# Kernel tuning notes

Hardware: AMD Instinct MI355X
Metric: run time of the kernel (lower is better)

The kernel has to match this reference:

```python
import jax, jax.numpy as jnp
import numpy as np

N = 100000   # nodes
E = 500000   # edges per relation
D = 128      # in_dim == out_dim
R = 3        # relations
NEG_SLOPE = 0.2  # DGL GATConv default


def setup_inputs() -> dict:
    key = jax.random.key(0)
    ks = jax.random.split(key, 7)
    x = jax.random.normal(ks[0], (N, D), jnp.float32)
    src = jax.random.randint(ks[1], (R, E), 0, N, jnp.int32)
    dst = jax.random.randint(ks[2], (R, E), 0, N, jnp.int32)
    W = jax.random.normal(ks[3], (R, D, D), jnp.float32) * 0.05
    attn_l = jax.random.normal(ks[4], (R, D), jnp.float32) * 0.05
    attn_r = jax.random.normal(ks[5], (R, D), jnp.float32) * 0.05
    bias = jnp.zeros((R, D), jnp.float32)
    return {"x": x, "src": src, "dst": dst, "W": W,
            "attn_l": attn_l, "attn_r": attn_r, "bias": bias}


def _gat_rel(x, src, dst, W, al, ar, b):
    # GATConv, num_heads=1: project, per-edge attention, segment softmax over dst
    feat = x @ W.T                                   # [N, D]
    el = (feat * al).sum(-1)                         # [N]
    er = (feat * ar).sum(-1)                         # [N]
    e = jax.nn.leaky_relu(el[src] + er[dst], NEG_SLOPE)   # [E]
    m = jax.ops.segment_max(e, dst, num_segments=N)       # stable softmax max per dst
    ex = jnp.exp(e - m[dst])
    s = jax.ops.segment_sum(ex, dst, num_segments=N)
    alpha = ex / s[dst]                                    # edge softmax weights
    out = jax.ops.segment_sum(alpha[:, None] * feat[src], dst, num_segments=N)
    return out + b                                         # GATConv bias


def reference(x, src, dst, W, attn_l, attn_r, bias):
    # HeteroGraphConv(aggregate='mean') over relations, then squeeze(head dim)
    outs = [_gat_rel(x, src[r], dst[r], W[r], attn_l[r], attn_r[r], bias[r])
            for r in range(R)]
    return jnp.mean(jnp.stack(outs, axis=0), axis=0)
```

## Files before the change

kernel.cpp:

```cpp
#include <hip/hip_runtime.h>
#include <hip/hip_bf16.h>

#define NN 100000
#define DD 128
#define RR 3
#define EE 500000
#define CAP 44
#define BK 196
#define ECAP 8192
#define SELR 50176

using bf16 = __hip_bfloat16;
typedef __attribute__((ext_vector_type(8))) short short8;
typedef __attribute__((ext_vector_type(4))) float f32x4;

__device__ __forceinline__ unsigned short f2bf(float f) {
  unsigned int u = __float_as_uint(f);
  return (unsigned short)((u + 0x7fffu + ((u >> 16) & 1u)) >> 16);
}
__device__ __forceinline__ float blo(unsigned int u) { return __uint_as_float(u << 16); }
__device__ __forceinline__ float bhi(unsigned int u) { return __uint_as_float(u & 0xffff0000u); }

__device__ __forceinline__ void ld_lds16(const void* g, void* l) {
  __builtin_amdgcn_global_load_lds((const __attribute__((address_space(1))) unsigned int*)g,
                                   (__attribute__((address_space(3))) unsigned int*)l, 16, 0, 0);
}

__global__ __launch_bounds__(256) void k_prepw(
    const float* __restrict__ W, const float* __restrict__ bias,
    short* __restrict__ Wb, float* __restrict__ bm)
{
  int idx = blockIdx.x * 256 + threadIdx.x;
  float4 v = ((const float4*)W)[idx];
  short4 s;
  s.x = (short)f2bf(v.x); s.y = (short)f2bf(v.y);
  s.z = (short)f2bf(v.z); s.w = (short)f2bf(v.w);
  ((short4*)Wb)[idx] = s;
  if (blockIdx.x == 0 && threadIdx.x < DD) {
    int t = threadIdx.x;
    bm[t] = (bias[t] + bias[DD + t] + bias[2 * DD + t]) * (1.f / 3.f);
  }
}

__global__ __launch_bounds__(256, 2) void k_gemm(
    const float* __restrict__ x, const short* __restrict__ Wb,
    const float* __restrict__ attn_l, const float* __restrict__ attn_r,
    short* __restrict__ feat, float* __restrict__ el, float* __restrict__ er)
{
  __shared__ __align__(16) char smem[65536];
  const int t = threadIdx.x, lane = t & 63, wave = t >> 6;
  const int row0 = blockIdx.x * 128;
  const int ml = lane & 15, q = lane >> 4;
  const int wr = wave >> 1, wc = wave & 1;

  {
    const int rbase = t >> 5, c4 = t & 31;
    const int chunk = c4 >> 1, half = c4 & 1;
    const int dst0 = ((chunk ^ (rbase & 7)) << 4) + (half << 3);
    const float4* x4 = (const float4*)x;
#pragma unroll 4
    for (int i = 0; i < 16; ++i) {
      int row = i * 8 + rbase;
      int grow = row0 + row; if (grow >= NN) grow = NN - 1;
      float4 v = x4[(size_t)grow * 32 + c4];
      unsigned int p0 = ((unsigned int)f2bf(v.y) << 16) | f2bf(v.x);
      unsigned int p1 = ((unsigned int)f2bf(v.w) << 16) | f2bf(v.z);
      *(uint2*)(smem + row * 256 + dst0) = make_uint2(p0, p1);
    }
  }

  int mbase[4], nbase[4];
#pragma unroll
  for (int i = 0; i < 4; ++i) {
    mbase[i] = (wr * 64 + i * 16 + ml) * 256;
    nbase[i] = 32768 + (wc * 64 + i * 16 + ml) * 256;
  }

  for (int rel = 0; rel < RR; ++rel) {
    if (rel) __syncthreads();
    {
      const int rloc = q & 3;
#pragma unroll
      for (int i = 0; i < 8; ++i) {
        int rowB = wave * 32 + i * 4 + rloc;
        int c = ml ^ (rowB & 7);
        const short* gp = Wb + (size_t)(rel * 128 + rowB) * 128 + c * 8;
        ld_lds16(gp, smem + 32768 + wave * 8192 + i * 1024);
      }
    }
    __syncthreads();

    f32x4 acc[4][4] = {};
#pragma unroll
    for (int kc = 0; kc < 4; ++kc) {
      const int sw = ((kc * 4 + q) ^ (ml & 7)) << 4;
      short8 av[4], bv[4];
#pragma unroll
      for (int i = 0; i < 4; ++i) av[i] = *(const short8*)(smem + mbase[i] + sw);
#pragma unroll
      for (int i = 0; i < 4; ++i) bv[i] = *(const short8*)(smem + nbase[i] + sw);
#pragma unroll
      for (int mi = 0; mi < 4; ++mi)
#pragma unroll
        for (int ni = 0; ni < 4; ++ni)
          acc[mi][ni] = __builtin_amdgcn_mfma_f32_16x16x32_bf16(av[mi], bv[ni], acc[mi][ni], 0, 0, 0);
    }

    float pel[4][4], per_[4][4];
    {
      float alv[4], arv[4];
#pragma unroll
      for (int ni = 0; ni < 4; ++ni) {
        int c = rel * DD + wc * 64 + ni * 16 + ml;
        alv[ni] = attn_l[c]; arv[ni] = attn_r[c];
      }
#pragma unroll
      for (int mi = 0; mi < 4; ++mi)
#pragma unroll
        for (int reg = 0; reg < 4; ++reg) {
          float se = 0.f, sr = 0.f;
#pragma unroll
          for (int ni = 0; ni < 4; ++ni) {
            se = fmaf(acc[mi][ni][reg], alv[ni], se);
            sr = fmaf(acc[mi][ni][reg], arv[ni], sr);
          }
          pel[mi][reg] = se; per_[mi][reg] = sr;
        }
#pragma unroll
      for (int msk = 1; msk < 16; msk <<= 1)
#pragma unroll
        for (int mi = 0; mi < 4; ++mi)
#pragma unroll
          for (int reg = 0; reg < 4; ++reg) {
            pel[mi][reg]  += __shfl_xor(pel[mi][reg], msk);
            per_[mi][reg] += __shfl_xor(per_[mi][reg], msk);
          }
    }

    char* fb = (char*)feat + (size_t)rel * NN * 256;
#pragma unroll
    for (int p = 0; p < 2; ++p) {
      __syncthreads();
      if (p == 0 && ml == 0) {
#pragma unroll
        for (int mi = 0; mi < 4; ++mi)
#pragma unroll
          for (int reg = 0; reg < 4; ++reg) {
            int row = wr * 64 + mi * 16 + q * 4 + reg;
            *(float*)(smem + SELR + row * 16 + wc * 4)     = pel[mi][reg];
            *(float*)(smem + SELR + row * 16 + 8 + wc * 4) = per_[mi][reg];
          }
      }
      if (wr == p) {
#pragma unroll
        for (int mi = 0; mi < 4; ++mi)
#pragma unroll
          for (int ni = 0; ni < 4; ++ni) {
            f32x4 v = acc[mi][ni];
#pragma unroll
            for (int reg = 0; reg < 4; ++reg) {
              int rl = mi * 16 + q * 4 + reg;
              *(short*)(smem + 32768 + rl * 272 + wc * 128 + ni * 32 + ml * 2) = (short)f2bf(v[reg]);
            }
          }
      }
      __syncthreads();
      if (p == 0 && t < 128 && row0 + t < NN) {
        float4 v = *(const float4*)(smem + SELR + t * 16);
        el[rel * NN + row0 + t] = v.x + v.y;
        er[rel * NN + row0 + t] = v.z + v.w;
      }
#pragma unroll
      for (int o = 0; o < 4; ++o) {
        int rl = o * 16 + (t >> 4);
        int coloff = (t & 15) * 16;
        int grow = row0 + p * 64 + rl;
        if (grow < NN) {
          int4 v = *(const int4*)(smem + 32768 + rl * 272 + coloff);
          *(int4*)(fb + (size_t)grow * 256 + coloff) = v;
        }
      }
    }
  }
}

__global__ __launch_bounds__(256) void k_part(
    const int* __restrict__ src, const int* __restrict__ dst,
    int* __restrict__ gcur, int* __restrict__ ebuf)
{
  __shared__ int lh[BK];
  const int t = threadIdx.x;
  for (int b = t; b < BK; b += 256) lh[b] = 0;
  __syncthreads();

  int eb[8], ebk[8];
  const int base = blockIdx.x * 2048 + t;
#pragma unroll
  for (int k = 0; k < 8; ++k) {
    int i = base + k * 256;
    ebk[k] = -1;
    if (i < RR * EE) {
      int d = __builtin_nontemporal_load(&dst[i]);
      int s = __builtin_nontemporal_load(&src[i]);
      int r = i >= 2 * EE ? 2 : (i >= EE ? 1 : 0);
      ebk[k] = d >> 9;
      eb[k] = ((d & 511) << 19) | (r << 17) | s;
      atomicAdd(&lh[ebk[k]], 1);
    }
  }
  __syncthreads();
  if (t < BK) {
    int v = lh[t];
    lh[t] = v ? atomicAdd(&gcur[t], v) : 0;
  }
  __syncthreads();
#pragma unroll
  for (int k = 0; k < 8; ++k) {
    if (ebk[k] >= 0) {
      int pos = atomicAdd(&lh[ebk[k]], 1);
      if (pos < ECAP) ebuf[ebk[k] * ECAP + pos] = eb[k];
    }
  }
}

__global__ __launch_bounds__(256) void k_build(
    const int* __restrict__ gcur, const int* __restrict__ ebuf,
    int* __restrict__ counts, int* __restrict__ payload)
{
  __shared__ int lcnt[512];
  const int b = blockIdx.x, t = threadIdx.x;
  lcnt[t] = 0; lcnt[t + 256] = 0;
  __syncthreads();
  int cnt = gcur[b]; if (cnt > ECAP) cnt = ECAP;
  const int n0 = b << 9;
  for (int i = t; i < cnt; i += 256) {
    int ent = ebuf[b * ECAP + i];
    int dlow = ent >> 19;
    int pos = atomicAdd(&lcnt[dlow], 1);
    if (pos < CAP)
      payload[(size_t)(n0 + dlow) * CAP + pos] = ((ent >> 17) & 3) * NN + (ent & 0x1FFFF);
  }
  __syncthreads();
  if (n0 + t < NN)       counts[n0 + t] = lcnt[t];
  if (n0 + t + 256 < NN) counts[n0 + t + 256] = lcnt[t + 256];
}

__global__ __launch_bounds__(256) void k_gather(
    const int* __restrict__ counts, const int* __restrict__ payload,
    const float* __restrict__ el, const float* __restrict__ er,
    const short* __restrict__ feat, const float* __restrict__ bm,
    float* __restrict__ out)
{
  const int lane = threadIdx.x & 63;
  const int hw = lane >> 4, m = lane & 15;
  const int n = blockIdx.x * 4 + (threadIdx.x >> 6);
  int deg = counts[n];
  deg = deg > CAP ? CAP : deg;
  const float er0 = er[n], er1 = er[NN + n], er2 = er[2 * NN + n];
  const bool act = lane < deg;
  int pl = act ? payload[(size_t)n * CAP + lane] : 0;
  int r = pl >= 2 * NN ? 2 : (pl >= NN ? 1 : 0);
  float ex = 0.f;
  if (act) {
    float e = el[pl] + (r == 0 ? er0 : (r == 1 ? er1 : er2));
    e = e >= 0.f ? e : 0.2f * e;
    ex = __expf(e);
  }
  float v0 = (act && r == 0) ? ex : 0.f;
  float v1 = (act && r == 1) ? ex : 0.f;
  float v2 = (act && r == 2) ? ex : 0.f;
#pragma unroll
  for (int msk = 1; msk < 64; msk <<= 1) {
    v0 += __shfl_xor(v0, msk);
    v1 += __shfl_xor(v1, msk);
    v2 += __shfl_xor(v2, msk);
  }
  float i0 = v0 > 0.f ? 1.f / v0 : 0.f;
  float i1 = v1 > 0.f ? 1.f / v1 : 0.f;
  float i2 = v2 > 0.f ? 1.f / v2 : 0.f;
  float w = ex * (r == 0 ? i0 : (r == 1 ? i1 : i2));

  float a8[8] = {0.f, 0.f, 0.f, 0.f, 0.f, 0.f, 0.f, 0.f};
  const unsigned short* fs = (const unsigned short*)feat;
  for (int e = 0; e < deg; e += 8) {
#pragma unroll
    for (int g = 0; g < 2; ++g) {
      int idx = e + g * 4 + hw;
      float we = __shfl(w, idx);
      int pe = __shfl(pl, idx);
      uint4 u = *(const uint4*)(fs + (size_t)pe * DD + m * 8);
      a8[0] = fmaf(we, blo(u.x), a8[0]); a8[1] = fmaf(we, bhi(u.x), a8[1]);
      a8[2] = fmaf(we, blo(u.y), a8[2]); a8[3] = fmaf(we, bhi(u.y), a8[3]);
      a8[4] = fmaf(we, blo(u.z), a8[4]); a8[5] = fmaf(we, bhi(u.z), a8[5]);
      a8[6] = fmaf(we, blo(u.w), a8[6]); a8[7] = fmaf(we, bhi(u.w), a8[7]);
    }
  }
#pragma unroll
  for (int k = 0; k < 8; ++k) {
    a8[k] += __shfl_xor(a8[k], 16);
    a8[k] += __shfl_xor(a8[k], 32);
  }
  if (hw == 0) {
    const int j = m * 8;
    float4 b0 = *(const float4*)(bm + j);
    float4 b1 = *(const float4*)(bm + j + 4);
    float4 o0, o1;
    o0.x = a8[0] * (1.f / 3.f) + b0.x; o0.y = a8[1] * (1.f / 3.f) + b0.y;
    o0.z = a8[2] * (1.f / 3.f) + b0.z; o0.w = a8[3] * (1.f / 3.f) + b0.w;
    o1.x = a8[4] * (1.f / 3.f) + b1.x; o1.y = a8[5] * (1.f / 3.f) + b1.y;
    o1.z = a8[6] * (1.f / 3.f) + b1.z; o1.w = a8[7] * (1.f / 3.f) + b1.w;
    float* op = out + (size_t)n * DD + j;
    *(float4*)op = o0;
    *(float4*)(op + 4) = o1;
  }
}

extern "C" void kernel_launch(void* const* d_in, const int* in_sizes, int n_in,
                              void* d_out, int out_size, void* d_ws, size_t ws_size,
                              hipStream_t stream)
{
  const float* x    = (const float*)d_in[0];
  const int*   src  = (const int*)d_in[1];
  const int*   dst  = (const int*)d_in[2];
  const float* W    = (const float*)d_in[3];
  const float* al   = (const float*)d_in[4];
  const float* ar   = (const float*)d_in[5];
  const float* bias = (const float*)d_in[6];
  float* out = (float*)d_out;

  char* p = (char*)d_ws;
  short* feat    = (short*)p; p += (size_t)RR * NN * DD * 2;
  int*   payload = (int*)p;   p += (size_t)NN * CAP * 4;
  int*   ebuf    = (int*)p;   p += (size_t)BK * ECAP * 4;
  float* el      = (float*)p; p += (size_t)RR * NN * 4;
  float* er      = (float*)p; p += (size_t)RR * NN * 4;
  short* Wb      = (short*)p; p += (size_t)RR * DD * DD * 2;
  float* bm      = (float*)p; p += (size_t)DD * 4;
  int*   counts  = (int*)p;   p += (size_t)NN * 4;
  int*   gcur    = (int*)p;   p += (size_t)BK * 4;

  hipMemsetAsync(gcur, 0, (size_t)BK * 4, stream);
  k_prepw<<<48, 256, 0, stream>>>(W, bias, Wb, bm);
  k_gemm<<<(NN + 127) / 128, 256, 0, stream>>>(x, Wb, al, ar, feat, el, er);
  k_part<<<(RR * EE + 2047) / 2048, 256, 0, stream>>>(src, dst, gcur, ebuf);
  k_build<<<BK, 256, 0, stream>>>(gcur, ebuf, counts, payload);
  k_gather<<<NN / 4, 256, 0, stream>>>(counts, payload, el, er, feat, bm, out);
}
```

Baseline: 266.3 us.

## Fuse GEMM and edge partition into one launch and fold memset into prep

Merges the projection GEMM and the edge bucketing kernel into a single launch, with block indices splitting the work between the two bodies, so independent work can overlap on the GPU. The gcur zeroing moves from a separate memset into the weight-prep kernel. This removes two launches and the idle tail between kernels. In exchange, partition blocks now carry the GEMM's 64KB shared allocation and launch bounds, which may lower their occupancy.

```diff
diff --git a/kernel.cpp b/kernel.cpp
--- a/kernel.cpp
+++ b/kernel.cpp
@@ -9,6 +9,8 @@
 #define BK 196
 #define ECAP 8192
 #define SELR 50176
+#define GEMM_NB 782
+#define PART_NB 733
 
 using bf16 = __hip_bfloat16;
 typedef __attribute__((ext_vector_type(8))) short short8;
@@ -26,9 +28,9 @@
                                    (__attribute__((address_space(3))) unsigned int*)l, 16, 0, 0);
 }
 
-__global__ __launch_bounds__(256) void k_prepw(
+__global__ __launch_bounds__(256) void k_pre(
     const float* __restrict__ W, const float* __restrict__ bias,
-    short* __restrict__ Wb, float* __restrict__ bm)
+    short* __restrict__ Wb, float* __restrict__ bm, int* __restrict__ gcur)
 {
   int idx = blockIdx.x * 256 + threadIdx.x;
   float4 v = ((const float4*)W)[idx];
@@ -40,16 +42,17 @@
     int t = threadIdx.x;
     bm[t] = (bias[t] + bias[DD + t] + bias[2 * DD + t]) * (1.f / 3.f);
   }
-}
-
-__global__ __launch_bounds__(256, 2) void k_gemm(
+  if (blockIdx.x == 1 && threadIdx.x < BK) gcur[threadIdx.x] = 0;
+}
+
+__device__ __forceinline__ void gemm_body(
+    char* smem, int bid,
     const float* __restrict__ x, const short* __restrict__ Wb,
     const float* __restrict__ attn_l, const float* __restrict__ attn_r,
     short* __restrict__ feat, float* __restrict__ el, float* __restrict__ er)
 {
-  __shared__ __align__(16) char smem[65536];
   const int t = threadIdx.x, lane = t & 63, wave = t >> 6;
-  const int row0 = blockIdx.x * 128;
+  const int row0 = bid * 128;
   const int ml = lane & 15, q = lane >> 4;
   const int wr = wave >> 1, wc = wave & 1;
 
@@ -184,17 +187,18 @@
   }
 }
 
-__global__ __launch_bounds__(256) void k_part(
+__device__ __forceinline__ void part_body(
+    char* smem, int vb,
     const int* __restrict__ src, const int* __restrict__ dst,
     int* __restrict__ gcur, int* __restrict__ ebuf)
 {
-  __shared__ int lh[BK];
+  int* lh = (int*)smem;
   const int t = threadIdx.x;
   for (int b = t; b < BK; b += 256) lh[b] = 0;
   __syncthreads();
 
   int eb[8], ebk[8];
-  const int base = blockIdx.x * 2048 + t;
+  const int base = vb * 2048 + t;
 #pragma unroll
   for (int k = 0; k < 8; ++k) {
     int i = base + k * 256;
@@ -220,6 +224,21 @@
       int pos = atomicAdd(&lh[ebk[k]], 1);
       if (pos < ECAP) ebuf[ebk[k] * ECAP + pos] = eb[k];
     }
+  }
+}
+
+__global__ __launch_bounds__(256, 2) void k_fused(
+    const float* __restrict__ x, const short* __restrict__ Wb,
+    const float* __restrict__ attn_l, const float* __restrict__ attn_r,
+    short* __restrict__ feat, float* __restrict__ el, float* __restrict__ er,
+    const int* __restrict__ src, const int* __restrict__ dst,
+    int* __restrict__ gcur, int* __restrict__ ebuf)
+{
+  __shared__ __align__(16) char smem[65536];
+  if (blockIdx.x < GEMM_NB) {
+    gemm_body(smem, blockIdx.x, x, Wb, attn_l, attn_r, feat, el, er);
+  } else {
+    part_body(smem, blockIdx.x - GEMM_NB, src, dst, gcur, ebuf);
   }
 }
 
@@ -339,10 +358,9 @@
   int*   counts  = (int*)p;   p += (size_t)NN * 4;
   int*   gcur    = (int*)p;   p += (size_t)BK * 4;
 
-  hipMemsetAsync(gcur, 0, (size_t)BK * 4, stream);
-  k_prepw<<<48, 256, 0, stream>>>(W, bias, Wb, bm);
-  k_gemm<<<(NN + 127) / 128, 256, 0, stream>>>(x, Wb, al, ar, feat, el, er);
-  k_part<<<(RR * EE + 2047) / 2048, 256, 0, stream>>>(src, dst, gcur, ebuf);
+  k_pre<<<48, 256, 0, stream>>>(W, bias, Wb, bm, gcur);
+  k_fused<<<GEMM_NB + PART_NB, 256, 0, stream>>>(x, Wb, al, ar, feat, el, er,
+                                                 src, dst, gcur, ebuf);
   k_build<<<BK, 256, 0, stream>>>(gcur, ebuf, counts, payload);
   k_gather<<<NN / 4, 256, 0, stream>>>(counts, payload, el, er, feat, bm, out);
 }
```

New measurement: 246.6 us. 1.08x faster.

## Aggregate raw x per relation before projecting, folding attention into weights

Applied to the files above, without the earlier changes.

Reorders the computation so each destination first aggregates raw fp32 x rows per relation (softmax weights per relation segment) into a bf16 buffer, then a single GEMM applies W over the three relations and adds the bias. The attention logits el/er come from precomputed W^T·attn vectors, which removes the initial projection GEMM. The el/er computation is fused with edge partitioning in one launch, gcur zeroing moves into the prep kernel, and the build kernel sorts edges by relation within each node. The gather now reads fp32 x rows (twice the bytes of the old bf16 feat) and writes a 3×N×D bf16 intermediate, trading gather bandwidth for fewer kernels and less GEMM work.

```diff
diff --git a/kernel.cpp b/kernel.cpp
--- a/kernel.cpp
+++ b/kernel.cpp
@@ -8,9 +8,10 @@
 #define CAP 44
 #define BK 196
 #define ECAP 8192
-#define SELR 50176
-
-using bf16 = __hip_bfloat16;
+#define GEMM_NB 782
+#define PART_NB 733
+#define PRE2_NB 256
+
 typedef __attribute__((ext_vector_type(8))) short short8;
 typedef __attribute__((ext_vector_type(4))) float f32x4;
 
@@ -18,17 +19,12 @@
   unsigned int u = __float_as_uint(f);
   return (unsigned short)((u + 0x7fffu + ((u >> 16) & 1u)) >> 16);
 }
-__device__ __forceinline__ float blo(unsigned int u) { return __uint_as_float(u << 16); }
-__device__ __forceinline__ float bhi(unsigned int u) { return __uint_as_float(u & 0xffff0000u); }
-
-__device__ __forceinline__ void ld_lds16(const void* g, void* l) {
-  __builtin_amdgcn_global_load_lds((const __attribute__((address_space(1))) unsigned int*)g,
-                                   (__attribute__((address_space(3))) unsigned int*)l, 16, 0, 0);
-}
-
-__global__ __launch_bounds__(256) void k_prepw(
+
+__global__ __launch_bounds__(256) void k_pre(
     const float* __restrict__ W, const float* __restrict__ bias,
-    short* __restrict__ Wb, float* __restrict__ bm)
+    const float* __restrict__ al, const float* __restrict__ ar,
+    short* __restrict__ Wb, float* __restrict__ bm,
+    float* __restrict__ wal, float* __restrict__ war, int* __restrict__ gcur)
 {
   int idx = blockIdx.x * 256 + threadIdx.x;
   float4 v = ((const float4*)W)[idx];
@@ -40,161 +36,75 @@
     int t = threadIdx.x;
     bm[t] = (bias[t] + bias[DD + t] + bias[2 * DD + t]) * (1.f / 3.f);
   }
-}
-
-__global__ __launch_bounds__(256, 2) void k_gemm(
-    const float* __restrict__ x, const short* __restrict__ Wb,
-    const float* __restrict__ attn_l, const float* __restrict__ attn_r,
-    short* __restrict__ feat, float* __restrict__ el, float* __restrict__ er)
-{
-  __shared__ __align__(16) char smem[65536];
-  const int t = threadIdx.x, lane = t & 63, wave = t >> 6;
-  const int row0 = blockIdx.x * 128;
-  const int ml = lane & 15, q = lane >> 4;
-  const int wr = wave >> 1, wc = wave & 1;
-
-  {
-    const int rbase = t >> 5, c4 = t & 31;
-    const int chunk = c4 >> 1, half = c4 & 1;
-    const int dst0 = ((chunk ^ (rbase & 7)) << 4) + (half << 3);
-    const float4* x4 = (const float4*)x;
-#pragma unroll 4
-    for (int i = 0; i < 16; ++i) {
-      int row = i * 8 + rbase;
-      int grow = row0 + row; if (grow >= NN) grow = NN - 1;
-      float4 v = x4[(size_t)grow * 32 + c4];
-      unsigned int p0 = ((unsigned int)f2bf(v.y) << 16) | f2bf(v.x);
-      unsigned int p1 = ((unsigned int)f2bf(v.w) << 16) | f2bf(v.z);
-      *(uint2*)(smem + row * 256 + dst0) = make_uint2(p0, p1);
-    }
-  }
-
-  int mbase[4], nbase[4];
-#pragma unroll
-  for (int i = 0; i < 4; ++i) {
-    mbase[i] = (wr * 64 + i * 16 + ml) * 256;
-    nbase[i] = 32768 + (wc * 64 + i * 16 + ml) * 256;
-  }
-
-  for (int rel = 0; rel < RR; ++rel) {
-    if (rel) __syncthreads();
-    {
-      const int rloc = q & 3;
-#pragma unroll
-      for (int i = 0; i < 8; ++i) {
-        int rowB = wave * 32 + i * 4 + rloc;
-        int c = ml ^ (rowB & 7);
-        const short* gp = Wb + (size_t)(rel * 128 + rowB) * 128 + c * 8;
-        ld_lds16(gp, smem + 32768 + wave * 8192 + i * 1024);
+  if (blockIdx.x == 1 && threadIdx.x < BK) gcur[threadIdx.x] = 0;
+  if (blockIdx.x == 2 && threadIdx.x < DD) {
+    int d = threadIdx.x;
+    float accl[RR] = {0.f, 0.f, 0.f}, accr[RR] = {0.f, 0.f, 0.f};
+    for (int i = 0; i < DD; ++i) {
+#pragma unroll
+      for (int r = 0; r < RR; ++r) {
+        float wv = W[(size_t)r * DD * DD + i * DD + d];
+        accl[r] = fmaf(wv, al[r * DD + i], accl[r]);
+        accr[r] = fmaf(wv, ar[r * DD + i], accr[r]);
       }
     }
-    __syncthreads();
-
-    f32x4 acc[4][4] = {};
-#pragma unroll
-    for (int kc = 0; kc < 4; ++kc) {
-      const int sw = ((kc * 4 + q) ^ (ml & 7)) << 4;
-      short8 av[4], bv[4];
-#pragma unroll
-      for (int i = 0; i < 4; ++i) av[i] = *(const short8*)(smem + mbase[i] + sw);
-#pragma unroll
-      for (int i = 0; i < 4; ++i) bv[i] = *(const short8*)(smem + nbase[i] + sw);
-#pragma unroll
-      for (int mi = 0; mi < 4; ++mi)
-#pragma unroll
-        for (int ni = 0; ni < 4; ++ni)
-          acc[mi][ni] = __builtin_amdgcn_mfma_f32_16x16x32_bf16(av[mi], bv[ni], acc[mi][ni], 0, 0, 0);
-    }
-
-    float pel[4][4], per_[4][4];
-    {
-      float alv[4], arv[4];
-#pragma unroll
-      for (int ni = 0; ni < 4; ++ni) {
-        int c = rel * DD + wc * 64 + ni * 16 + ml;
-        alv[ni] = attn_l[c]; arv[ni] = attn_r[c];
+#pragma unroll
+    for (int r = 0; r < RR; ++r) { wal[r * DD + d] = accl[r]; war[r * DD + d] = accr[r]; }
+  }
+}
+
+__device__ __forceinline__ void pre2_body(
+    int vb, const float* __restrict__ x,
+    const float* __restrict__ wal, const float* __restrict__ war,
+    float* __restrict__ el, float* __restrict__ er)
+{
+  const int t = threadIdx.x;
+  const int rowslot = t >> 5, lane32 = t & 31;
+  float4 wl[RR], wr2[RR];
+#pragma unroll
+  for (int r = 0; r < RR; ++r) {
+    wl[r]  = *(const float4*)(wal + r * DD + lane32 * 4);
+    wr2[r] = *(const float4*)(war + r * DD + lane32 * 4);
+  }
+  const int rpb = (NN + PRE2_NB - 1) / PRE2_NB;
+  int rbeg = vb * rpb;
+  int rend = rbeg + rpb; if (rend > NN) rend = NN;
+  for (int row = rbeg + rowslot; row < rend; row += 8) {
+    float4 xv = *(const float4*)(x + (size_t)row * DD + lane32 * 4);
+    float pl_[RR], pr_[RR];
+#pragma unroll
+    for (int r = 0; r < RR; ++r) {
+      pl_[r] = fmaf(xv.w, wl[r].w, fmaf(xv.z, wl[r].z, fmaf(xv.y, wl[r].y, xv.x * wl[r].x)));
+      pr_[r] = fmaf(xv.w, wr2[r].w, fmaf(xv.z, wr2[r].z, fmaf(xv.y, wr2[r].y, xv.x * wr2[r].x)));
+    }
+#pragma unroll
+    for (int msk = 1; msk < 32; msk <<= 1)
+#pragma unroll
+      for (int r = 0; r < RR; ++r) {
+        pl_[r] += __shfl_xor(pl_[r], msk);
+        pr_[r] += __shfl_xor(pr_[r], msk);
       }
-#pragma unroll
-      for (int mi = 0; mi < 4; ++mi)
-#pragma unroll
-        for (int reg = 0; reg < 4; ++reg) {
-          float se = 0.f, sr = 0.f;
-#pragma unroll
-          for (int ni = 0; ni < 4; ++ni) {
-            se = fmaf(acc[mi][ni][reg], alv[ni], se);
-            sr = fmaf(acc[mi][ni][reg], arv[ni], sr);
-          }
-          pel[mi][reg] = se; per_[mi][reg] = sr;
-        }
-#pragma unroll
-      for (int msk = 1; msk < 16; msk <<= 1)
-#pragma unroll
-        for (int mi = 0; mi < 4; ++mi)
-#pragma unroll
-          for (int reg = 0; reg < 4; ++reg) {
-            pel[mi][reg]  += __shfl_xor(pel[mi][reg], msk);
-            per_[mi][reg] += __shfl_xor(per_[mi][reg], msk);
-          }
-    }
-
-    char* fb = (char*)feat + (size_t)rel * NN * 256;
-#pragma unroll
-    for (int p = 0; p < 2; ++p) {
-      __syncthreads();
-      if (p == 0 && ml == 0) {
-#pragma unroll
-        for (int mi = 0; mi < 4; ++mi)
-#pragma unroll
-          for (int reg = 0; reg < 4; ++reg) {
-            int row = wr * 64 + mi * 16 + q * 4 + reg;
-            *(float*)(smem + SELR + row * 16 + wc * 4)     = pel[mi][reg];
-            *(float*)(smem + SELR + row * 16 + 8 + wc * 4) = per_[mi][reg];
-          }
+    if (lane32 == 0) {
+#pragma unroll
+      for (int r = 0; r < RR; ++r) {
+        el[r * NN + row] = pl_[r];
+        er[r * NN + row] = pr_[r];
       }
-      if (wr == p) {
-#pragma unroll
-        for (int mi = 0; mi < 4; ++mi)
-#pragma unroll
-          for (int ni = 0; ni < 4; ++ni) {
-            f32x4 v = acc[mi][ni];
-#pragma unroll
-            for (int reg = 0; reg < 4; ++reg) {
-              int rl = mi * 16 + q * 4 + reg;
-              *(short*)(smem + 32768 + rl * 272 + wc * 128 + ni * 32 + ml * 2) = (short)f2bf(v[reg]);
-            }
-          }
-      }
-      __syncthreads();
-      if (p == 0 && t < 128 && row0 + t < NN) {
-        float4 v = *(const float4*)(smem + SELR + t * 16);
-        el[rel * NN + row0 + t] = v.x + v.y;
-        er[rel * NN + row0 + t] = v.z + v.w;
-      }
-#pragma unroll
-      for (int o = 0; o < 4; ++o) {
-        int rl = o * 16 + (t >> 4);
-        int coloff = (t & 15) * 16;
-        int grow = row0 + p * 64 + rl;
-        if (grow < NN) {
-          int4 v = *(const int4*)(smem + 32768 + rl * 272 + coloff);
-          *(int4*)(fb + (size_t)grow * 256 + coloff) = v;
-        }
-      }
-    }
-  }
-}
-
-__global__ __launch_bounds__(256) void k_part(
+    }
+  }
+}
+
+__device__ __forceinline__ void part_body(
+    int* lh, int vb,
     const int* __restrict__ src, const int* __restrict__ dst,
     int* __restrict__ gcur, int* __restrict__ ebuf)
 {
-  __shared__ int lh[BK];
   const int t = threadIdx.x;
   for (int b = t; b < BK; b += 256) lh[b] = 0;
   __syncthreads();
 
   int eb[8], ebk[8];
-  const int base = blockIdx.x * 2048 + t;
+  const int base = vb * 2048 + t;
 #pragma unroll
   for (int k = 0; k < 8; ++k) {
     int i = base + k * 256;
@@ -223,46 +133,71 @@
   }
 }
 
-__global__ __launch_bounds__(256) void k_build(
+__global__ __launch_bounds__(256) void k_fused6(
+    const float* __restrict__ x, const float* __restrict__ wal,
+    const float* __restrict__ war, float* __restrict__ el, float* __restrict__ er,
+    const int* __restrict__ src, const int* __restrict__ dst,
+    int* __restrict__ gcur, int* __restrict__ ebuf)
+{
+  __shared__ int lh[BK];
+  if (blockIdx.x < PRE2_NB) {
+    pre2_body(blockIdx.x, x, wal, war, el, er);
+  } else {
+    part_body(lh, blockIdx.x - PRE2_NB, src, dst, gcur, ebuf);
+  }
+}
+
+__global__ __launch_bounds__(256) void k_build2(
     const int* __restrict__ gcur, const int* __restrict__ ebuf,
     int* __restrict__ counts, int* __restrict__ payload)
 {
-  __shared__ int lcnt[512];
+  __shared__ int lc[512 * 3];
   const int b = blockIdx.x, t = threadIdx.x;
-  lcnt[t] = 0; lcnt[t + 256] = 0;
+#pragma unroll
+  for (int i = 0; i < 6; ++i) lc[t + i * 256] = 0;
   __syncthreads();
   int cnt = gcur[b]; if (cnt > ECAP) cnt = ECAP;
   const int n0 = b << 9;
   for (int i = t; i < cnt; i += 256) {
     int ent = ebuf[b * ECAP + i];
-    int dlow = ent >> 19;
-    int pos = atomicAdd(&lcnt[dlow], 1);
+    atomicAdd(&lc[(ent >> 19) * 3 + ((ent >> 17) & 3)], 1);
+  }
+  __syncthreads();
+  for (int nl = t; nl < 512; nl += 256) {
+    int c0 = lc[nl * 3], c1 = lc[nl * 3 + 1], c2 = lc[nl * 3 + 2];
+    if (n0 + nl < NN) counts[n0 + nl] = c0 | (c1 << 8) | (c2 << 16);
+    lc[nl * 3]     = 0;
+    lc[nl * 3 + 1] = c0;
+    lc[nl * 3 + 2] = c0 + c1;
+  }
+  __syncthreads();
+  for (int i = t; i < cnt; i += 256) {
+    int ent = ebuf[b * ECAP + i];
+    int nl = ent >> 19;
+    int pos = atomicAdd(&lc[nl * 3 + ((ent >> 17) & 3)], 1);
     if (pos < CAP)
-      payload[(size_t)(n0 + dlow) * CAP + pos] = ((ent >> 17) & 3) * NN + (ent & 0x1FFFF);
-  }
-  __syncthreads();
-  if (n0 + t < NN)       counts[n0 + t] = lcnt[t];
-  if (n0 + t + 256 < NN) counts[n0 + t + 256] = lcnt[t + 256];
-}
-
-__global__ __launch_bounds__(256) void k_gather(
+      payload[(size_t)(n0 + nl) * CAP + pos] = ent & 0x7FFFF;
+  }
+}
+
+__global__ __launch_bounds__(256) void k_gather2(
     const int* __restrict__ counts, const int* __restrict__ payload,
     const float* __restrict__ el, const float* __restrict__ er,
-    const short* __restrict__ feat, const float* __restrict__ bm,
-    float* __restrict__ out)
+    const float* __restrict__ x, short* __restrict__ agg)
 {
   const int lane = threadIdx.x & 63;
   const int hw = lane >> 4, m = lane & 15;
   const int n = blockIdx.x * 4 + (threadIdx.x >> 6);
-  int deg = counts[n];
-  deg = deg > CAP ? CAP : deg;
+  int c3 = counts[n];
+  int d0 = c3 & 255, d1 = (c3 >> 8) & 255, d2 = (c3 >> 16) & 255;
+  int deg = d0 + d1 + d2; if (deg > CAP) deg = CAP;
   const float er0 = er[n], er1 = er[NN + n], er2 = er[2 * NN + n];
   const bool act = lane < deg;
   int pl = act ? payload[(size_t)n * CAP + lane] : 0;
-  int r = pl >= 2 * NN ? 2 : (pl >= NN ? 1 : 0);
+  int r = pl >> 17;
   float ex = 0.f;
   if (act) {
-    float e = el[pl] + (r == 0 ? er0 : (r == 1 ? er1 : er2));
+    float e = el[r * NN + (pl & 0x1FFFF)] + (r == 0 ? er0 : (r == 1 ? er1 : er2));
     e = e >= 0.f ? e : 0.2f * e;
     ex = __expf(e);
   }
@@ -280,39 +215,108 @@
   float i2 = v2 > 0.f ? 1.f / v2 : 0.f;
   float w = ex * (r == 0 ? i0 : (r == 1 ? i1 : i2));
 
-  float a8[8] = {0.f, 0.f, 0.f, 0.f, 0.f, 0.f, 0.f, 0.f};
-  const unsigned short* fs = (const unsigned short*)feat;
-  for (int e = 0; e < deg; e += 8) {
-#pragma unroll
-    for (int g = 0; g < 2; ++g) {
-      int idx = e + g * 4 + hw;
-      float we = __shfl(w, idx);
-      int pe = __shfl(pl, idx);
-      uint4 u = *(const uint4*)(fs + (size_t)pe * DD + m * 8);
-      a8[0] = fmaf(we, blo(u.x), a8[0]); a8[1] = fmaf(we, bhi(u.x), a8[1]);
-      a8[2] = fmaf(we, blo(u.y), a8[2]); a8[3] = fmaf(we, bhi(u.y), a8[3]);
-      a8[4] = fmaf(we, blo(u.z), a8[4]); a8[5] = fmaf(we, bhi(u.z), a8[5]);
-      a8[6] = fmaf(we, blo(u.w), a8[6]); a8[7] = fmaf(we, bhi(u.w), a8[7]);
-    }
-  }
-#pragma unroll
-  for (int k = 0; k < 8; ++k) {
-    a8[k] += __shfl_xor(a8[k], 16);
-    a8[k] += __shfl_xor(a8[k], 32);
-  }
-  if (hw == 0) {
-    const int j = m * 8;
-    float4 b0 = *(const float4*)(bm + j);
-    float4 b1 = *(const float4*)(bm + j + 4);
-    float4 o0, o1;
-    o0.x = a8[0] * (1.f / 3.f) + b0.x; o0.y = a8[1] * (1.f / 3.f) + b0.y;
-    o0.z = a8[2] * (1.f / 3.f) + b0.z; o0.w = a8[3] * (1.f / 3.f) + b0.w;
-    o1.x = a8[4] * (1.f / 3.f) + b1.x; o1.y = a8[5] * (1.f / 3.f) + b1.y;
-    o1.z = a8[6] * (1.f / 3.f) + b1.z; o1.w = a8[7] * (1.f / 3.f) + b1.w;
-    float* op = out + (size_t)n * DD + j;
-    *(float4*)op = o0;
-    *(float4*)(op + 4) = o1;
-  }
+#define SEG(SB, SD, R)                                                      \
+  {                                                                         \
+    float a8[8] = {0.f, 0.f, 0.f, 0.f, 0.f, 0.f, 0.f, 0.f};                 \
+    for (int e = 0; e < (SD); e += 16) {                                    \
+      _Pragma("unroll")                                                     \
+      for (int g = 0; g < 4; ++g) {                                         \
+        int li = e + g * 4 + hw;                                            \
+        int idx = (SB) + li;                                                \
+        float we = __shfl(w, idx);                                          \
+        we = li < (SD) ? we : 0.f;                                          \
+        int pe = __shfl(pl, idx) & 0x1FFFF;                                 \
+        const float* rp = x + (size_t)pe * DD + m * 8;                      \
+        float4 f0 = *(const float4*)rp;                                     \
+        float4 f1 = *(const float4*)(rp + 4);                               \
+        a8[0] = fmaf(we, f0.x, a8[0]); a8[1] = fmaf(we, f0.y, a8[1]);       \
+        a8[2] = fmaf(we, f0.z, a8[2]); a8[3] = fmaf(we, f0.w, a8[3]);       \
+        a8[4] = fmaf(we, f1.x, a8[4]); a8[5] = fmaf(we, f1.y, a8[5]);       \
+        a8[6] = fmaf(we, f1.z, a8[6]); a8[7] = fmaf(we, f1.w, a8[7]);       \
+      }                                                                     \
+    }                                                                       \
+    _Pragma("unroll")                                                       \
+    for (int k = 0; k < 8; ++k) {                                           \
+      a8[k] += __shfl_xor(a8[k], 16);                                       \
+      a8[k] += __shfl_xor(a8[k], 32);                                       \
+    }                                                                       \
+    if (hw == 0) {                                                          \
+      uint4 o;                                                              \
+      o.x = (unsigned)f2bf(a8[0]) | ((unsigned)f2bf(a8[1]) << 16);          \
+      o.y = (unsigned)f2bf(a8[2]) | ((unsigned)f2bf(a8[3]) << 16);          \
+      o.z = (unsigned)f2bf(a8[4]) | ((unsigned)f2bf(a8[5]) << 16);          \
+      o.w = (unsigned)f2bf(a8[6]) | ((unsigned)f2bf(a8[7]) << 16);          \
+      *(uint4*)((char*)agg + ((size_t)n * 3 + (R)) * 256 + m * 16) = o;     \
+    }                                                                       \
+  }
+
+  SEG(0, d0, 0)
+  SEG(d0, d1, 1)
+  SEG(d0 + d1, d2, 2)
+#undef SEG
+}
+
+__global__ __launch_bounds__(256, 2) void k_gemm2(
+    const short* __restrict__ agg, const short* __restrict__ Wb,
+    const float* __restrict__ bm, float* __restrict__ out)
+{
+  __shared__ __align__(16) char smem[65536];
+  const int t = threadIdx.x, lane = t & 63, wave = t >> 6;
+  const int ml = lane & 15, q = lane >> 4;
+  const int wr = wave >> 1, wc = wave & 1;
+  const int row0 = blockIdx.x * 128;
+
+  int mbase[4], nbase[4];
+#pragma unroll
+  for (int i = 0; i < 4; ++i) {
+    mbase[i] = (wr * 64 + i * 16 + ml) * 256;
+    nbase[i] = 32768 + (wc * 64 + i * 16 + ml) * 256;
+  }
+
+  f32x4 acc[4][4] = {};
+  for (int rel = 0; rel < RR; ++rel) {
+    if (rel) __syncthreads();
+#pragma unroll
+    for (int rnd = 0; rnd < 8; ++rnd) {
+      int row = (t >> 4) + rnd * 16;
+      int c = t & 15;
+      int grow = row0 + row; if (grow >= NN) grow = NN - 1;
+      uint4 va = *(const uint4*)(agg + ((size_t)grow * 3 + rel) * 128 + c * 8);
+      *(uint4*)(smem + row * 256 + ((c ^ (row & 7)) << 4)) = va;
+      uint4 vb = *(const uint4*)(Wb + (size_t)(rel * 128 + row) * 128 + c * 8);
+      *(uint4*)(smem + 32768 + row * 256 + ((c ^ (row & 7)) << 4)) = vb;
+    }
+    __syncthreads();
+#pragma unroll
+    for (int kc = 0; kc < 4; ++kc) {
+      const int sw = ((kc * 4 + q) ^ (ml & 7)) << 4;
+      short8 av[4], bv[4];
+#pragma unroll
+      for (int i = 0; i < 4; ++i) av[i] = *(const short8*)(smem + mbase[i] + sw);
+#pragma unroll
+      for (int i = 0; i < 4; ++i) bv[i] = *(const short8*)(smem + nbase[i] + sw);
+#pragma unroll
+      for (int mi = 0; mi < 4; ++mi)
+#pragma unroll
+        for (int ni = 0; ni < 4; ++ni)
+          acc[mi][ni] = __builtin_amdgcn_mfma_f32_16x16x32_bf16(av[mi], bv[ni], acc[mi][ni], 0, 0, 0);
+    }
+  }
+  float bmv[4];
+#pragma unroll
+  for (int ni = 0; ni < 4; ++ni) bmv[ni] = bm[wc * 64 + ni * 16 + ml];
+#pragma unroll
+  for (int mi = 0; mi < 4; ++mi)
+#pragma unroll
+    for (int ni = 0; ni < 4; ++ni) {
+      f32x4 v = acc[mi][ni];
+#pragma unroll
+      for (int reg = 0; reg < 4; ++reg) {
+        int grow = row0 + wr * 64 + mi * 16 + q * 4 + reg;
+        if (grow < NN)
+          out[(size_t)grow * DD + wc * 64 + ni * 16 + ml] = v[reg] * (1.f / 3.f) + bmv[ni];
+      }
+    }
 }
 
 extern "C" void kernel_launch(void* const* d_in, const int* in_sizes, int n_in,
@@ -329,20 +333,22 @@
   float* out = (float*)d_out;
 
   char* p = (char*)d_ws;
-  short* feat    = (short*)p; p += (size_t)RR * NN * DD * 2;
+  short* agg     = (short*)p; p += (size_t)NN * RR * DD * 2;
   int*   payload = (int*)p;   p += (size_t)NN * CAP * 4;
   int*   ebuf    = (int*)p;   p += (size_t)BK * ECAP * 4;
   float* el      = (float*)p; p += (size_t)RR * NN * 4;
   float* er      = (float*)p; p += (size_t)RR * NN * 4;
   short* Wb      = (short*)p; p += (size_t)RR * DD * DD * 2;
   float* bm      = (float*)p; p += (size_t)DD * 4;
+  float* wal     = (float*)p; p += (size_t)RR * DD * 4;
+  float* war     = (float*)p; p += (size_t)RR * DD * 4;
   int*   counts  = (int*)p;   p += (size_t)NN * 4;
   int*   gcur    = (int*)p;   p += (size_t)BK * 4;
 
-  hipMemsetAsync(gcur, 0, (size_t)BK * 4, stream);
-  k_prepw<<<48, 256, 0, stream>>>(W, bias, Wb, bm);
-  k_gemm<<<(NN + 127) / 128, 256, 0, stream>>>(x, Wb, al, ar, feat, el, er);
-  k_part<<<(RR * EE + 2047) / 2048, 256, 0, stream>>>(src, dst, gcur, ebuf);
-  k_build<<<BK, 256, 0, stream>>>(gcur, ebuf, counts, payload);
-  k_gather<<<NN / 4, 256, 0, stream>>>(counts, payload, el, er, feat, bm, out);
-}
+  k_pre<<<48, 256, 0, stream>>>(W, bias, al, ar, Wb, bm, wal, war, gcur);
+  k_fused6<<<PRE2_NB + PART_NB, 256, 0, stream>>>(x, wal, war, el, er,
+                                                  src, dst, gcur, ebuf);
+  k_build2<<<BK, 256, 0, stream>>>(gcur, ebuf, counts, payload);
+  k_gather2<<<NN / 4, 256, 0, stream>>>(counts, payload, el, er, x, agg);
+  k_gemm2<<<GEMM_NB, 256, 0, stream>>>(agg, Wb, bm, out);
+}
```

Result: slower. 362.2 us (+36.0%).
